# Optimization experiments

Hardware: AMD Instinct MI355X
Metric: run time of the kernel (lower is better)

## Reference

```python
import jax, jax.numpy as jnp
import numpy as np
from jax import lax

DIM = 128
HEADS = 8
HEAD_DIM = DIM // HEADS
SR = 2
B, H, W = 2, 80, 80
SCALE = HEAD_DIM ** (-0.5)
BN_EPS = 1e-5


def _conv1x1(x, w, b):
    # x: (B,C,H,W), w: (O,C), b: (O,)
    return jnp.einsum('bchw,oc->bohw', x, w) + b[None, :, None, None]


def setup_inputs() -> dict:
    key = jax.random.key(0)
    ks = jax.random.split(key, 12)
    s = DIM ** -0.5
    x = jax.random.normal(ks[0], (B, DIM, H, W), dtype=jnp.float32)
    q_w = jax.random.normal(ks[1], (DIM, DIM), dtype=jnp.float32) * s
    q_b = jnp.zeros((DIM,), jnp.float32)
    k_w = jax.random.normal(ks[2], (DIM, DIM), dtype=jnp.float32) * s
    k_b = jnp.zeros((DIM,), jnp.float32)
    v_w = jax.random.normal(ks[3], (DIM, DIM), dtype=jnp.float32) * s
    v_b = jnp.zeros((DIM,), jnp.float32)
    sr_w = jax.random.normal(ks[4], (DIM, DIM, SR, SR), dtype=jnp.float32) * (s / SR)
    sr_b = jnp.zeros((DIM,), jnp.float32)
    bn_gamma = jnp.ones((DIM,), jnp.float32)
    bn_beta = jnp.zeros((DIM,), jnp.float32)
    bn_mean = jnp.zeros((DIM,), jnp.float32)
    bn_var = jnp.ones((DIM,), jnp.float32)
    proj_w = jax.random.normal(ks[5], (DIM, DIM), dtype=jnp.float32) * s
    proj_b = jnp.zeros((DIM,), jnp.float32)
    return dict(x=x, q_w=q_w, q_b=q_b, k_w=k_w, k_b=k_b, v_w=v_w, v_b=v_b,
                sr_w=sr_w, sr_b=sr_b, bn_gamma=bn_gamma, bn_beta=bn_beta,
                bn_mean=bn_mean, bn_var=bn_var, proj_w=proj_w, proj_b=proj_b)


def reference(x, q_w, q_b, k_w, k_b, v_w, v_b, sr_w, sr_b,
              bn_gamma, bn_beta, bn_mean, bn_var, proj_w, proj_b):
    b, c, h, w = x.shape
    n = h * w
    # q: (B,h,N,d)
    q = _conv1x1(x, q_w, q_b).reshape(b, HEADS, HEAD_DIM, n).transpose(0, 1, 3, 2)
    # spatial reduction: Conv2d(k=SR, s=SR) + BN(eval) + ReLU
    x_kv = lax.conv_general_dilated(x, sr_w, window_strides=(SR, SR),
                                    padding='VALID',
                                    dimension_numbers=('NCHW', 'OIHW', 'NCHW'))
    x_kv = x_kv + sr_b[None, :, None, None]
    inv = bn_gamma / jnp.sqrt(bn_var + BN_EPS)
    x_kv = x_kv * inv[None, :, None, None] + (bn_beta - bn_mean * inv)[None, :, None, None]
    x_kv = jax.nn.relu(x_kv)
    n_kv = x_kv.shape[2] * x_kv.shape[3]
    k = _conv1x1(x_kv, k_w, k_b).reshape(b, HEADS, HEAD_DIM, n_kv).transpose(0, 1, 3, 2)
    v = _conv1x1(x_kv, v_w, v_b).reshape(b, HEADS, HEAD_DIM, n_kv).transpose(0, 1, 3, 2)
    # explicit attention: (B,h,N,N_kv)
    attn = jnp.einsum('bhnd,bhmd->bhnm', q, k) * SCALE
    attn = jax.nn.softmax(attn, axis=-1)
    out = jnp.einsum('bhnm,bhmd->bhnd', attn, v)  # (B,h,N,d)
    # faithful to source layout: transpose(1,2) then reshape to (B,C,H,W)
    out = out.transpose(0, 2, 1, 3).reshape(b, c, h, w)
    out = _conv1x1(out, proj_w, proj_b)
    return out
```

## Files before the change

### kernel.cpp

```cpp
#include <hip/hip_runtime.h>
#include <hip/hip_bf16.h>
#include <cmath>

#define DIM 128
#define HEADS 8
#define NBATCH 2
#define NQ 6400
#define NKV 1600
#define NC 50
#define NSPLIT 2
#define CPS 25
#define BN_EPS 1e-5f
#define LOG2E 1.4426950408889634f

typedef __bf16 bf16_t;
typedef __attribute__((ext_vector_type(8))) __bf16 bf16x8;
typedef __attribute__((ext_vector_type(16))) float f32x16;

union BF8U { bf16x8 v; unsigned u[4]; };

__device__ inline unsigned packbf2(float a, float b) {
  union { __hip_bfloat162 v; unsigned u; } r;
  r.v = __float22bfloat162_rn(make_float2(a, b));
  return r.u;
}

__device__ inline unsigned short f2bf(float v) {
  unsigned u = __float_as_uint(v);
  return (unsigned short)((u + 0x7FFFu + ((u >> 16) & 1u)) >> 16);
}

__global__ __launch_bounds__(256) void wcast(
    const float* __restrict__ qw, const float* __restrict__ kw,
    const float* __restrict__ vw, const float* __restrict__ pw,
    const float* __restrict__ srw, unsigned short* __restrict__ Wb)
{
  int e4 = (blockIdx.x * 256 + threadIdx.x) * 4;
  const float* src; int idx;
  if (e4 < 16384)      { src = qw;  idx = e4; }
  else if (e4 < 32768) { src = kw;  idx = e4 - 16384; }
  else if (e4 < 49152) { src = vw;  idx = e4 - 32768; }
  else if (e4 < 65536) { src = pw;  idx = e4 - 49152; }
  else                 { src = srw; idx = e4 - 65536; }
  float4 v = *(const float4*)(src + idx);
  uint2 wv;
  wv.x = packbf2(v.x, v.y);
  wv.y = packbf2(v.z, v.w);
  *(uint2*)&Wb[e4] = wv;
}

__global__ __launch_bounds__(256) void mgemm_qsrkv(
    const float* __restrict__ x, const bf16_t* __restrict__ Wb,
    const float* __restrict__ q_b, const float* __restrict__ sr_b,
    const float* __restrict__ k_b, const float* __restrict__ v_b,
    const float* __restrict__ bng, const float* __restrict__ bnb,
    const float* __restrict__ bnm, const float* __restrict__ bnv,
    unsigned short* __restrict__ Qb,
    unsigned short* __restrict__ Kp, unsigned short* __restrict__ Vp,
    float sl)
{
  __shared__ __align__(16) unsigned short xs4[32][520];
  __shared__ __align__(16) unsigned short xs[32][136];
  int t = threadIdx.x;
  int ln = t & 31, hf = (t >> 5) & 1, wid = t >> 6;
  int b = blockIdx.y;
  int o = wid * 32 + ln;

  if (blockIdx.x < 50) {
    int cid = blockIdx.x;
    int s0 = cid * 32;

    {
      int tx = t & 31, g = t >> 5;
      int s = s0 + tx;
      int i = s / 40, j = s % 40;
      const float* xb = x + (size_t)b * DIM * NQ;
#pragma unroll
      for (int u = 0; u < 32; ++u) {
        int idx2 = g * 32 + u;
        int c = idx2 >> 1, ky = idx2 & 1;
        const float* src = xb + (size_t)c * NQ + (2 * i + ky) * 80 + 2 * j;
        float2 vv = *(const float2*)src;
        *(unsigned*)&xs4[tx][c * 4 + ky * 2] = packbf2(vv.x, vv.y);
      }
    }
    __syncthreads();

    const unsigned short* arow = &xs4[ln][hf * 8];
    const bf16_t* brow = &Wb[65536 + (size_t)o * 512 + hf * 8];
    f32x16 acc = {};
#pragma unroll 8
    for (int c0 = 0; c0 < 512; c0 += 16) {
      bf16x8 af = *(const bf16x8*)&arow[c0];
      bf16x8 bf = *(const bf16x8*)&brow[c0];
      acc = __builtin_amdgcn_mfma_f32_32x32x16_bf16(af, bf, acc, 0, 0, 0);
    }
    float bv = sr_b[o];
    float inv = bng[o] / sqrtf(bnv[o] + BN_EPS);
    float b2 = bnb[o] - bnm[o] * inv;
#pragma unroll
    for (int g = 0; g < 4; ++g)
#pragma unroll
      for (int jj = 0; jj < 4; ++jj) {
        int sr = 8 * g + 4 * hf + jj;
        xs[sr][o] = f2bf(fmaxf((acc[4 * g + jj] + bv) * inv + b2, 0.f));
      }
    __syncthreads();

    const unsigned short* ar2 = &xs[ln][hf * 8];
    const bf16_t* kbrow = &Wb[16384 + (size_t)o * DIM + hf * 8];
    const bf16_t* vbrow = &Wb[32768 + (size_t)o * DIM + hf * 8];
    f32x16 ka = {}, va = {};
#pragma unroll
    for (int c0 = 0; c0 < 128; c0 += 16) {
      bf16x8 af = *(const bf16x8*)&ar2[c0];
      bf16x8 kb = *(const bf16x8*)&kbrow[c0];
      bf16x8 vb = *(const bf16x8*)&vbrow[c0];
      ka = __builtin_amdgcn_mfma_f32_32x32x16_bf16(af, kb, ka, 0, 0, 0);
      va = __builtin_amdgcn_mfma_f32_32x32x16_bf16(af, vb, va, 0, 0, 0);
    }
    int hloc = o >> 4, d = o & 15;
    {
      float kb2 = k_b[o];
      size_t CB = (((size_t)b * HEADS + hloc) * NC + cid) * 512;
#pragma unroll
      for (int g = 0; g < 4; ++g)
#pragma unroll
        for (int jj = 0; jj < 4; ++jj) {
          int sl2 = 8 * g + 4 * hf + jj;
          Kp[CB + sl2 * 16 + d] = f2bf(ka[4 * g + jj] + kb2);
        }
    }
    {
      float vb2 = v_b[o];
      size_t CB = (((size_t)b * HEADS + hloc) * NC + cid) * 1024;
      uint4 w0, w1;
      w0.x = packbf2(va[0] + vb2, va[1] + vb2);
      w0.y = packbf2(va[2] + vb2, va[3] + vb2);
      w0.z = packbf2(va[4] + vb2, va[5] + vb2);
      w0.w = packbf2(va[6] + vb2, va[7] + vb2);
      w1.x = packbf2(va[8] + vb2, va[9] + vb2);
      w1.y = packbf2(va[10] + vb2, va[11] + vb2);
      w1.z = packbf2(va[12] + vb2, va[13] + vb2);
      w1.w = packbf2(va[14] + vb2, va[15] + vb2);
      *(uint4*)&Vp[CB + d * 16 + hf * 8] = w0;
      *(uint4*)&Vp[CB + 512 + d * 16 + hf * 8] = w1;
    }
    {
      int hh = t >> 5, pos = t & 31;
      size_t addr = (((size_t)b * HEADS + hh) * NC + cid) * 1024 + 256 +
                    ((pos & 16) ? 512 : 0) + (pos & 15);
      Vp[addr] = 0x3F80;
    }
  } else {
    int s0 = (blockIdx.x - 50) * 32;

    {
      int tx = t & 31, cg = t >> 5;
      const float* xb = x + (size_t)b * DIM * NQ + s0 + tx;
#pragma unroll
      for (int it = 0; it < 8; ++it) {
        int c = 2 * cg + 16 * it;
        float a0 = xb[(size_t)c * NQ];
        float a1 = xb[(size_t)(c + 1) * NQ];
        *(unsigned*)&xs[tx][c] = packbf2(a0, a1);
      }
    }
    __syncthreads();

    const unsigned short* arow = &xs[ln][hf * 8];
    const bf16_t* brow = &Wb[(size_t)o * DIM + hf * 8];
    f32x16 acc = {};
#pragma unroll
    for (int c0 = 0; c0 < 128; c0 += 16) {
      bf16x8 af = *(const bf16x8*)&arow[c0];
      bf16x8 bf = *(const bf16x8*)&brow[c0];
      acc = __builtin_amdgcn_mfma_f32_32x32x16_bf16(af, bf, acc, 0, 0, 0);
    }
    float bv = q_b[o];
#pragma unroll
    for (int g = 0; g < 4; ++g)
#pragma unroll
      for (int jj = 0; jj < 4; ++jj) {
        int sq = s0 + 8 * g + 4 * hf + jj;
        Qb[((size_t)b * NQ + sq) * DIM + o] = f2bf((acc[4 * g + jj] + bv) * sl);
      }
  }
}

__global__ __launch_bounds__(256) void attn_split(
    const bf16_t* __restrict__ Qb, const bf16_t* __restrict__ Kp,
    const bf16_t* __restrict__ Vp, unsigned short* __restrict__ Pb,
    float* __restrict__ Lsum)
{
  __shared__ __align__(16) unsigned short ldsK[2][512];
  __shared__ __align__(16) unsigned short ldsV[2][1024];

  const int t = threadIdx.x;
  const int ln = t & 31, hf = (t >> 5) & 1, wid = t >> 6;
  const int h = blockIdx.y;
  const int b = blockIdx.z & 1, sp = blockIdx.z >> 1;
  const int q0 = blockIdx.x * 128 + wid * 32;

  bf16x8 qf = *(const bf16x8*)&Qb[((size_t)b * NQ + q0 + ln) * DIM + h * 16 + hf * 8];
  const int bh = b * HEADS + h;
  const bf16_t* kcg = &Kp[((size_t)bh * NC + sp * CPS) * 512];
  const bf16_t* vcg = &Vp[((size_t)bh * NC + sp * CPS) * 1024];

  if (t < 64)       *(uint4*)&ldsK[0][t * 8] = *(const uint4*)&kcg[t * 8];
  else if (t < 192) *(uint4*)&ldsV[0][(t - 64) * 8] = *(const uint4*)&vcg[(t - 64) * 8];
  __syncthreads();

  f32x16 acc0 = {}, acc1 = {};
  const f32x16 zero = {};

  for (int c = 0; c < CPS; ++c) {
    const int cb = c & 1;
    uint4 tmp;
    if (c + 1 < CPS) {
      if (t < 64)       tmp = *(const uint4*)&kcg[(size_t)(c + 1) * 512 + t * 8];
      else if (t < 192) tmp = *(const uint4*)&vcg[(size_t)(c + 1) * 1024 + (t - 64) * 8];
    }

    bf16x8 kf = *(const bf16x8*)&ldsK[cb][ln * 16 + hf * 8];
    f32x16 S = __builtin_amdgcn_mfma_f32_32x32x16_bf16(kf, qf, zero, 0, 0, 0);

    BF8U f0, f1;
#pragma unroll
    for (int i = 0; i < 4; ++i) {
      f0.u[i] = packbf2(__builtin_amdgcn_exp2f(S[2 * i]),
                        __builtin_amdgcn_exp2f(S[2 * i + 1]));
      f1.u[i] = packbf2(__builtin_amdgcn_exp2f(S[8 + 2 * i]),
                        __builtin_amdgcn_exp2f(S[9 + 2 * i]));
    }

    bf16x8 va = *(const bf16x8*)&ldsV[cb][ln * 16 + hf * 8];
    bf16x8 vb = *(const bf16x8*)&ldsV[cb][512 + ln * 16 + hf * 8];
    acc0 = __builtin_amdgcn_mfma_f32_32x32x16_bf16(va, f0.v, acc0, 0, 0, 0);
    acc1 = __builtin_amdgcn_mfma_f32_32x32x16_bf16(vb, f1.v, acc1, 0, 0, 0);

    if (c + 1 < CPS) {
      if (t < 64)       *(uint4*)&ldsK[cb ^ 1][t * 8] = tmp;
      else if (t < 192) *(uint4*)&ldsV[cb ^ 1][(t - 64) * 8] = tmp;
    }
    __syncthreads();
  }

  f32x16 acc;
#pragma unroll
  for (int i = 0; i < 16; ++i) acc[i] = acc0[i] + acc1[i];

  unsigned short* prow =
      &Pb[(size_t)(sp * 2 + b) * (NQ * DIM) + (size_t)(q0 + ln) * DIM + h * 16 + 4 * hf];
  uint2 w0, w1;
  w0.x = packbf2(acc[0], acc[1]); w0.y = packbf2(acc[2], acc[3]);
  w1.x = packbf2(acc[4], acc[5]); w1.y = packbf2(acc[6], acc[7]);
  *(uint2*)&prow[0] = w0;
  *(uint2*)&prow[8] = w1;
  if (!hf)
    Lsum[(size_t)(sp * 2 + b) * (HEADS * NQ) + (size_t)h * NQ + q0 + ln] = acc[8];
}

__global__ __launch_bounds__(256) void proj_comb(
    const unsigned short* __restrict__ Pb, const float* __restrict__ Lsum,
    const bf16_t* __restrict__ Wb, const float* __restrict__ p_b,
    float* __restrict__ Out)
{
  __shared__ __align__(16) unsigned short As[32][136];
  int t = threadIdx.x;
  int b = blockIdx.y;
  int s0 = blockIdx.x * 32;

  {
    int tp = t & 15, cg = t >> 4;
#pragma unroll
    for (int it = 0; it < 8; ++it) {
      int c = cg * 8 + it;
      int f = c * NQ + s0 + 2 * tp;
      int n = f >> 7, hh = (f >> 4) & 7;
      float plo = 0.f, phi = 0.f, L = 0.f;
#pragma unroll
      for (int s = 0; s < NSPLIT; ++s) {
        unsigned u = *(const unsigned*)&Pb[(size_t)(2 * s + b) * (NQ * DIM) + f];
        plo += __uint_as_float(u << 16);
        phi += __uint_as_float(u & 0xFFFF0000u);
        L += Lsum[(size_t)(2 * s + b) * (HEADS * NQ) + (size_t)hh * NQ + n];
      }
      As[2 * tp][c]     = f2bf(plo / L);
      As[2 * tp + 1][c] = f2bf(phi / L);
    }
  }
  __syncthreads();

  int ln = t & 31, hf = (t >> 5) & 1, wid = t >> 6;
  int o = wid * 32 + ln;
  const bf16_t* brow = &Wb[49152 + (size_t)o * DIM + hf * 8];
  const unsigned short* arow = &As[ln][hf * 8];
  f32x16 acc = {};
#pragma unroll
  for (int c0 = 0; c0 < 128; c0 += 16) {
    bf16x8 af = *(const bf16x8*)&arow[c0];
    bf16x8 bf = *(const bf16x8*)&brow[c0];
    acc = __builtin_amdgcn_mfma_f32_32x32x16_bf16(af, bf, acc, 0, 0, 0);
  }
  float bv = p_b[o];
  float* obase = &Out[((size_t)b * DIM + o) * NQ + s0 + 4 * hf];
#pragma unroll
  for (int g = 0; g < 4; ++g) {
    float4 r;
    r.x = acc[4 * g + 0] + bv; r.y = acc[4 * g + 1] + bv;
    r.z = acc[4 * g + 2] + bv; r.w = acc[4 * g + 3] + bv;
    *(float4*)&obase[8 * g] = r;
  }
}

extern "C" void kernel_launch(void* const* d_in, const int* in_sizes, int n_in,
                              void* d_out, int out_size, void* d_ws, size_t ws_size,
                              hipStream_t stream)
{
  const float* x    = (const float*)d_in[0];
  const float* q_w  = (const float*)d_in[1];
  const float* q_b  = (const float*)d_in[2];
  const float* k_w  = (const float*)d_in[3];
  const float* k_b  = (const float*)d_in[4];
  const float* v_w  = (const float*)d_in[5];
  const float* v_b  = (const float*)d_in[6];
  const float* sr_w = (const float*)d_in[7];
  const float* sr_b = (const float*)d_in[8];
  const float* bng  = (const float*)d_in[9];
  const float* bnb  = (const float*)d_in[10];
  const float* bnm  = (const float*)d_in[11];
  const float* bnv  = (const float*)d_in[12];
  const float* p_w  = (const float*)d_in[13];
  const float* p_b  = (const float*)d_in[14];
  float* out = (float*)d_out;

  float* ws = (float*)d_ws;
  bf16_t* Qb   = (bf16_t*)(ws);
  bf16_t* Kp   = (bf16_t*)(ws + 819200);
  bf16_t* Vp   = (bf16_t*)(ws + 1024000);
  float*  Lsum = ws + 1433600;
  bf16_t* Pb   = (bf16_t*)(ws + 1945600);
  bf16_t* Wb   = (bf16_t*)(ws + 6041600);

  const float sl = 0.25f * LOG2E;

  wcast<<<dim3(128), dim3(256), 0, stream>>>(
      q_w, k_w, v_w, p_w, sr_w, (unsigned short*)Wb);

  mgemm_qsrkv<<<dim3(250, NBATCH), dim3(256), 0, stream>>>(
      x, Wb, q_b, sr_b, k_b, v_b, bng, bnb, bnm, bnv,
      (unsigned short*)Qb, (unsigned short*)Kp, (unsigned short*)Vp, sl);

  attn_split<<<dim3(NQ / 128, HEADS, 2 * NSPLIT), dim3(256), 0, stream>>>(
      Qb, Kp, Vp, (unsigned short*)Pb, Lsum);

  proj_comb<<<dim3(200, NBATCH), dim3(256), 0, stream>>>(
      (const unsigned short*)Pb, Lsum, Wb, p_b, out);
}
```

Before: 156.9 us.

## Load K/V fragments directly from global into registers with two-chunk software pipeline

Drops the LDS double-buffered K/V staging and per-chunk __syncthreads in the attention kernel. Each lane now loads its K and V fragments straight from global memory into registers, prefetching two chunks ahead with an unrolled A/B ping-pong. It also merges the two accumulators into one dependent MFMA chain. The aim is to remove barrier and LDS round-trip overhead, at the cost of redundant global loads across the four waves (relying on L1/L2 hits) and a longer serial MFMA dependency chain.

```diff
diff --git a/kernel.cpp b/kernel.cpp
--- a/kernel.cpp
+++ b/kernel.cpp
@@ -193,9 +193,6 @@
     const bf16_t* __restrict__ Vp, unsigned short* __restrict__ Pb,
     float* __restrict__ Lsum)
 {
-  __shared__ __align__(16) unsigned short ldsK[2][512];
-  __shared__ __align__(16) unsigned short ldsV[2][1024];
-
   const int t = threadIdx.x;
   const int ln = t & 31, hf = (t >> 5) & 1, wid = t >> 6;
   const int h = blockIdx.y;
@@ -204,51 +201,64 @@
 
   bf16x8 qf = *(const bf16x8*)&Qb[((size_t)b * NQ + q0 + ln) * DIM + h * 16 + hf * 8];
   const int bh = b * HEADS + h;
-  const bf16_t* kcg = &Kp[((size_t)bh * NC + sp * CPS) * 512];
-  const bf16_t* vcg = &Vp[((size_t)bh * NC + sp * CPS) * 1024];
-
-  if (t < 64)       *(uint4*)&ldsK[0][t * 8] = *(const uint4*)&kcg[t * 8];
-  else if (t < 192) *(uint4*)&ldsV[0][(t - 64) * 8] = *(const uint4*)&vcg[(t - 64) * 8];
-  __syncthreads();
-
-  f32x16 acc0 = {}, acc1 = {};
+  const bf16_t* kc = &Kp[((size_t)bh * NC + sp * CPS) * 512 + ln * 16 + hf * 8];
+  const bf16_t* vc = &Vp[((size_t)bh * NC + sp * CPS) * 1024 + ln * 16 + hf * 8];
+
+  f32x16 acc = {};
   const f32x16 zero = {};
 
-  for (int c = 0; c < CPS; ++c) {
-    const int cb = c & 1;
-    uint4 tmp;
-    if (c + 1 < CPS) {
-      if (t < 64)       tmp = *(const uint4*)&kcg[(size_t)(c + 1) * 512 + t * 8];
-      else if (t < 192) tmp = *(const uint4*)&vcg[(size_t)(c + 1) * 1024 + (t - 64) * 8];
-    }
-
-    bf16x8 kf = *(const bf16x8*)&ldsK[cb][ln * 16 + hf * 8];
-    f32x16 S = __builtin_amdgcn_mfma_f32_32x32x16_bf16(kf, qf, zero, 0, 0, 0);
-
+  bf16x8 kA  = *(const bf16x8*)kc;
+  bf16x8 vaA = *(const bf16x8*)vc;
+  bf16x8 vbA = *(const bf16x8*)(vc + 512);
+  bf16x8 kB  = *(const bf16x8*)(kc + 512);
+  bf16x8 vaB = *(const bf16x8*)(vc + 1024);
+  bf16x8 vbB = *(const bf16x8*)(vc + 1536);
+
+  for (int i = 0; i < 12; ++i) {
+    f32x16 S = __builtin_amdgcn_mfma_f32_32x32x16_bf16(kA, qf, zero, 0, 0, 0);
+    kA = *(const bf16x8*)(kc + (size_t)(2 * i + 2) * 512);
     BF8U f0, f1;
 #pragma unroll
-    for (int i = 0; i < 4; ++i) {
-      f0.u[i] = packbf2(__builtin_amdgcn_exp2f(S[2 * i]),
-                        __builtin_amdgcn_exp2f(S[2 * i + 1]));
-      f1.u[i] = packbf2(__builtin_amdgcn_exp2f(S[8 + 2 * i]),
-                        __builtin_amdgcn_exp2f(S[9 + 2 * i]));
-    }
-
-    bf16x8 va = *(const bf16x8*)&ldsV[cb][ln * 16 + hf * 8];
-    bf16x8 vb = *(const bf16x8*)&ldsV[cb][512 + ln * 16 + hf * 8];
-    acc0 = __builtin_amdgcn_mfma_f32_32x32x16_bf16(va, f0.v, acc0, 0, 0, 0);
-    acc1 = __builtin_amdgcn_mfma_f32_32x32x16_bf16(vb, f1.v, acc1, 0, 0, 0);
-
-    if (c + 1 < CPS) {
-      if (t < 64)       *(uint4*)&ldsK[cb ^ 1][t * 8] = tmp;
-      else if (t < 192) *(uint4*)&ldsV[cb ^ 1][(t - 64) * 8] = tmp;
-    }
-    __syncthreads();
-  }
-
-  f32x16 acc;
-#pragma unroll
-  for (int i = 0; i < 16; ++i) acc[i] = acc0[i] + acc1[i];
+    for (int j = 0; j < 4; ++j) {
+      f0.u[j] = packbf2(__builtin_amdgcn_exp2f(S[2 * j]),
+                        __builtin_amdgcn_exp2f(S[2 * j + 1]));
+      f1.u[j] = packbf2(__builtin_amdgcn_exp2f(S[8 + 2 * j]),
+                        __builtin_amdgcn_exp2f(S[9 + 2 * j]));
+    }
+    acc = __builtin_amdgcn_mfma_f32_32x32x16_bf16(vaA, f0.v, acc, 0, 0, 0);
+    acc = __builtin_amdgcn_mfma_f32_32x32x16_bf16(vbA, f1.v, acc, 0, 0, 0);
+    vaA = *(const bf16x8*)(vc + (size_t)(2 * i + 2) * 1024);
+    vbA = *(const bf16x8*)(vc + (size_t)(2 * i + 2) * 1024 + 512);
+
+    int c3 = (2 * i + 3 < CPS) ? 2 * i + 3 : CPS - 1;
+    f32x16 T = __builtin_amdgcn_mfma_f32_32x32x16_bf16(kB, qf, zero, 0, 0, 0);
+    kB = *(const bf16x8*)(kc + (size_t)c3 * 512);
+    BF8U g0, g1;
+#pragma unroll
+    for (int j = 0; j < 4; ++j) {
+      g0.u[j] = packbf2(__builtin_amdgcn_exp2f(T[2 * j]),
+                        __builtin_amdgcn_exp2f(T[2 * j + 1]));
+      g1.u[j] = packbf2(__builtin_amdgcn_exp2f(T[8 + 2 * j]),
+                        __builtin_amdgcn_exp2f(T[9 + 2 * j]));
+    }
+    acc = __builtin_amdgcn_mfma_f32_32x32x16_bf16(vaB, g0.v, acc, 0, 0, 0);
+    acc = __builtin_amdgcn_mfma_f32_32x32x16_bf16(vbB, g1.v, acc, 0, 0, 0);
+    vaB = *(const bf16x8*)(vc + (size_t)c3 * 1024);
+    vbB = *(const bf16x8*)(vc + (size_t)c3 * 1024 + 512);
+  }
+  {
+    f32x16 S = __builtin_amdgcn_mfma_f32_32x32x16_bf16(kA, qf, zero, 0, 0, 0);
+    BF8U f0, f1;
+#pragma unroll
+    for (int j = 0; j < 4; ++j) {
+      f0.u[j] = packbf2(__builtin_amdgcn_exp2f(S[2 * j]),
+                        __builtin_amdgcn_exp2f(S[2 * j + 1]));
+      f1.u[j] = packbf2(__builtin_amdgcn_exp2f(S[8 + 2 * j]),
+                        __builtin_amdgcn_exp2f(S[9 + 2 * j]));
+    }
+    acc = __builtin_amdgcn_mfma_f32_32x32x16_bf16(vaA, f0.v, acc, 0, 0, 0);
+    acc = __builtin_amdgcn_mfma_f32_32x32x16_bf16(vbA, f1.v, acc, 0, 0, 0);
+  }
 
   unsigned short* prow =
       &Pb[(size_t)(sp * 2 + b) * (NQ * DIM) + (size_t)(q0 + ln) * DIM + h * 16 + 4 * hf];
```

Result: faster. 145.2 us (-7.4%).

## Split KV chunks across waves within block and reduce in LDS, drop split-K combine

Applied to the files above, without the earlier changes.

The attention kernel now gives each block 32 queries and spreads the 50 KV chunks across its four waves. Each wave reads K/V fragments straight from global memory, and the partial accumulators and row sums are reduced through shared memory, with normalization done in-kernel. This removes the global split-K partial buffers, the Lsum array, the LDS double buffering and barriers, and the combine pass in the projection kernel, so the projection now just loads normalized bf16 rows. In exchange, each block re-reads all of K/V for only 32 queries. That raises global and L2 traffic, and the loads are no longer staged through LDS.

```diff
diff --git a/kernel.cpp b/kernel.cpp
--- a/kernel.cpp
+++ b/kernel.cpp
@@ -8,8 +8,6 @@
 #define NQ 6400
 #define NKV 1600
 #define NC 50
-#define NSPLIT 2
-#define CPS 25
 #define BN_EPS 1e-5f
 #define LOG2E 1.4426950408889634f
 
@@ -188,83 +186,73 @@
   }
 }
 
-__global__ __launch_bounds__(256) void attn_split(
+__global__ __launch_bounds__(256) void attn_full(
     const bf16_t* __restrict__ Qb, const bf16_t* __restrict__ Kp,
-    const bf16_t* __restrict__ Vp, unsigned short* __restrict__ Pb,
-    float* __restrict__ Lsum)
-{
-  __shared__ __align__(16) unsigned short ldsK[2][512];
-  __shared__ __align__(16) unsigned short ldsV[2][1024];
+    const bf16_t* __restrict__ Vp, unsigned short* __restrict__ Pb)
+{
+  __shared__ float R[4][9][64];
 
   const int t = threadIdx.x;
   const int ln = t & 31, hf = (t >> 5) & 1, wid = t >> 6;
   const int h = blockIdx.y;
-  const int b = blockIdx.z & 1, sp = blockIdx.z >> 1;
-  const int q0 = blockIdx.x * 128 + wid * 32;
+  const int b = blockIdx.z;
+  const int q0 = blockIdx.x * 32;
 
   bf16x8 qf = *(const bf16x8*)&Qb[((size_t)b * NQ + q0 + ln) * DIM + h * 16 + hf * 8];
   const int bh = b * HEADS + h;
-  const bf16_t* kcg = &Kp[((size_t)bh * NC + sp * CPS) * 512];
-  const bf16_t* vcg = &Vp[((size_t)bh * NC + sp * CPS) * 1024];
-
-  if (t < 64)       *(uint4*)&ldsK[0][t * 8] = *(const uint4*)&kcg[t * 8];
-  else if (t < 192) *(uint4*)&ldsV[0][(t - 64) * 8] = *(const uint4*)&vcg[(t - 64) * 8];
+  const bf16_t* kc = &Kp[(size_t)bh * NC * 512 + ln * 16 + hf * 8];
+  const bf16_t* vc = &Vp[(size_t)bh * NC * 1024 + ln * 16 + hf * 8];
+
+  f32x16 acc = {};
+  const f32x16 zero = {};
+
+  for (int c = wid; c < NC; c += 4) {
+    bf16x8 kf = *(const bf16x8*)(kc + (size_t)c * 512);
+    bf16x8 va = *(const bf16x8*)(vc + (size_t)c * 1024);
+    bf16x8 vb = *(const bf16x8*)(vc + (size_t)c * 1024 + 512);
+
+    f32x16 S = __builtin_amdgcn_mfma_f32_32x32x16_bf16(kf, qf, zero, 0, 0, 0);
+    BF8U f0, f1;
+#pragma unroll
+    for (int j = 0; j < 4; ++j) {
+      f0.u[j] = packbf2(__builtin_amdgcn_exp2f(S[2 * j]),
+                        __builtin_amdgcn_exp2f(S[2 * j + 1]));
+      f1.u[j] = packbf2(__builtin_amdgcn_exp2f(S[8 + 2 * j]),
+                        __builtin_amdgcn_exp2f(S[9 + 2 * j]));
+    }
+    acc = __builtin_amdgcn_mfma_f32_32x32x16_bf16(va, f0.v, acc, 0, 0, 0);
+    acc = __builtin_amdgcn_mfma_f32_32x32x16_bf16(vb, f1.v, acc, 0, 0, 0);
+  }
+
+#pragma unroll
+  for (int r = 0; r < 9; ++r) R[wid][r][t & 63] = acc[r];
   __syncthreads();
 
-  f32x16 acc0 = {}, acc1 = {};
-  const f32x16 zero = {};
-
-  for (int c = 0; c < CPS; ++c) {
-    const int cb = c & 1;
-    uint4 tmp;
-    if (c + 1 < CPS) {
-      if (t < 64)       tmp = *(const uint4*)&kcg[(size_t)(c + 1) * 512 + t * 8];
-      else if (t < 192) tmp = *(const uint4*)&vcg[(size_t)(c + 1) * 1024 + (t - 64) * 8];
-    }
-
-    bf16x8 kf = *(const bf16x8*)&ldsK[cb][ln * 16 + hf * 8];
-    f32x16 S = __builtin_amdgcn_mfma_f32_32x32x16_bf16(kf, qf, zero, 0, 0, 0);
-
-    BF8U f0, f1;
-#pragma unroll
-    for (int i = 0; i < 4; ++i) {
-      f0.u[i] = packbf2(__builtin_amdgcn_exp2f(S[2 * i]),
-                        __builtin_amdgcn_exp2f(S[2 * i + 1]));
-      f1.u[i] = packbf2(__builtin_amdgcn_exp2f(S[8 + 2 * i]),
-                        __builtin_amdgcn_exp2f(S[9 + 2 * i]));
-    }
-
-    bf16x8 va = *(const bf16x8*)&ldsV[cb][ln * 16 + hf * 8];
-    bf16x8 vb = *(const bf16x8*)&ldsV[cb][512 + ln * 16 + hf * 8];
-    acc0 = __builtin_amdgcn_mfma_f32_32x32x16_bf16(va, f0.v, acc0, 0, 0, 0);
-    acc1 = __builtin_amdgcn_mfma_f32_32x32x16_bf16(vb, f1.v, acc1, 0, 0, 0);
-
-    if (c + 1 < CPS) {
-      if (t < 64)       *(uint4*)&ldsK[cb ^ 1][t * 8] = tmp;
-      else if (t < 192) *(uint4*)&ldsV[cb ^ 1][(t - 64) * 8] = tmp;
-    }
-    __syncthreads();
-  }
-
-  f32x16 acc;
-#pragma unroll
-  for (int i = 0; i < 16; ++i) acc[i] = acc0[i] + acc1[i];
-
-  unsigned short* prow =
-      &Pb[(size_t)(sp * 2 + b) * (NQ * DIM) + (size_t)(q0 + ln) * DIM + h * 16 + 4 * hf];
-  uint2 w0, w1;
-  w0.x = packbf2(acc[0], acc[1]); w0.y = packbf2(acc[2], acc[3]);
-  w1.x = packbf2(acc[4], acc[5]); w1.y = packbf2(acc[6], acc[7]);
-  *(uint2*)&prow[0] = w0;
-  *(uint2*)&prow[8] = w1;
-  if (!hf)
-    Lsum[(size_t)(sp * 2 + b) * (HEADS * NQ) + (size_t)h * NQ + q0 + ln] = acc[8];
-}
-
-__global__ __launch_bounds__(256) void proj_comb(
-    const unsigned short* __restrict__ Pb, const float* __restrict__ Lsum,
-    const bf16_t* __restrict__ Wb, const float* __restrict__ p_b,
-    float* __restrict__ Out)
+  if (wid == 0) {
+    int l64 = t & 63;
+    float s[9];
+#pragma unroll
+    for (int r = 0; r < 9; ++r)
+      s[r] = R[0][r][l64] + R[1][r][l64] + R[2][r][l64] + R[3][r][l64];
+    float L = hf ? (R[0][8][ln] + R[1][8][ln] + R[2][8][ln] + R[3][8][ln])
+                 : s[8];
+    float inv = __builtin_amdgcn_rcpf(L);
+
+    unsigned short* prow =
+        &Pb[(size_t)b * (NQ * DIM) + (size_t)(q0 + ln) * DIM + h * 16 + 4 * hf];
+    uint2 w0, w1;
+    w0.x = packbf2(s[0] * inv, s[1] * inv);
+    w0.y = packbf2(s[2] * inv, s[3] * inv);
+    w1.x = packbf2(s[4] * inv, s[5] * inv);
+    w1.y = packbf2(s[6] * inv, s[7] * inv);
+    *(uint2*)&prow[0] = w0;
+    *(uint2*)&prow[8] = w1;
+  }
+}
+
+__global__ __launch_bounds__(256) void proj(
+    const unsigned short* __restrict__ Pb, const bf16_t* __restrict__ Wb,
+    const float* __restrict__ p_b, float* __restrict__ Out)
 {
   __shared__ __align__(16) unsigned short As[32][136];
   int t = threadIdx.x;
@@ -273,21 +261,14 @@
 
   {
     int tp = t & 15, cg = t >> 4;
+    const unsigned short* pbase = Pb + (size_t)b * (NQ * DIM);
 #pragma unroll
     for (int it = 0; it < 8; ++it) {
       int c = cg * 8 + it;
       int f = c * NQ + s0 + 2 * tp;
-      int n = f >> 7, hh = (f >> 4) & 7;
-      float plo = 0.f, phi = 0.f, L = 0.f;
-#pragma unroll
-      for (int s = 0; s < NSPLIT; ++s) {
-        unsigned u = *(const unsigned*)&Pb[(size_t)(2 * s + b) * (NQ * DIM) + f];
-        plo += __uint_as_float(u << 16);
-        phi += __uint_as_float(u & 0xFFFF0000u);
-        L += Lsum[(size_t)(2 * s + b) * (HEADS * NQ) + (size_t)hh * NQ + n];
-      }
-      As[2 * tp][c]     = f2bf(plo / L);
-      As[2 * tp + 1][c] = f2bf(phi / L);
+      unsigned u = *(const unsigned*)&pbase[f];
+      As[2 * tp][c]     = (unsigned short)(u & 0xFFFFu);
+      As[2 * tp + 1][c] = (unsigned short)(u >> 16);
     }
   }
   __syncthreads();
@@ -339,9 +320,8 @@
   bf16_t* Qb   = (bf16_t*)(ws);
   bf16_t* Kp   = (bf16_t*)(ws + 819200);
   bf16_t* Vp   = (bf16_t*)(ws + 1024000);
-  float*  Lsum = ws + 1433600;
-  bf16_t* Pb   = (bf16_t*)(ws + 1945600);
-  bf16_t* Wb   = (bf16_t*)(ws + 6041600);
+  bf16_t* Pb   = (bf16_t*)(ws + 1433600);
+  bf16_t* Wb   = (bf16_t*)(ws + 2252800);
 
   const float sl = 0.25f * LOG2E;
 
@@ -352,9 +332,9 @@
       x, Wb, q_b, sr_b, k_b, v_b, bng, bnb, bnm, bnv,
       (unsigned short*)Qb, (unsigned short*)Kp, (unsigned short*)Vp, sl);
 
-  attn_split<<<dim3(NQ / 128, HEADS, 2 * NSPLIT), dim3(256), 0, stream>>>(
-      Qb, Kp, Vp, (unsigned short*)Pb, Lsum);
-
-  proj_comb<<<dim3(200, NBATCH), dim3(256), 0, stream>>>(
-      (const unsigned short*)Pb, Lsum, Wb, p_b, out);
-}
+  attn_full<<<dim3(NQ / 32, HEADS, NBATCH), dim3(256), 0, stream>>>(
+      Qb, Kp, Vp, (unsigned short*)Pb);
+
+  proj<<<dim3(200, NBATCH), dim3(256), 0, stream>>>(
+      (const unsigned short*)Pb, Wb, p_b, out);
+}
```

After: 137.8 us. -12.2%, faster.
